# Kernel optimization log

Hardware: AMD Instinct MI355X
Metric: run time of the kernel (lower is better)

Reference implementation:

```python
import jax, jax.numpy as jnp
import numpy as np

H = 14
N = H * H
DIM = 768
INT = 5
LAM = 3.5


def fft_conv_grouped(x, w):
    # x: (B, g*in_c, N) real; w: (g, int_c, in_c, H, H//2+1) complex
    g, int_c, in_c = w.shape[:3]
    B = x.shape[0]
    xf = jnp.fft.rfftn(x.reshape(B, g, in_c, H, H), axes=(-2, -1), norm='ortho')
    yf = jnp.einsum('bgchf,gichf->bgihf', xf, w)
    y = jnp.fft.irfftn(yf, s=(H, H), axes=(-2, -1), norm='ortho')
    return y.reshape(B, g * int_c, N)


def soft(x, t):
    # sign(x) * relu(|x| - t)
    return jnp.sign(x) * jnp.maximum(jnp.abs(x) - t, 0.0)


def batch_norm(x, gamma, beta, eps=1e-5):
    # training-mode BatchNorm1d applied per channel over (B, N); x: (B, N, C)
    m = x.mean(axis=(0, 1))
    v = x.var(axis=(0, 1))
    return (x - m) * jax.lax.rsqrt(v + eps) * gamma + beta


def setup_inputs() -> dict:
    key = jax.random.key(0)
    ks = jax.random.split(key, 8)
    B = 32
    Hf = H // 2 + 1
    # kernel: init randn*0.06, then normalize_parameters()
    kr = jax.random.normal(ks[0], (DIM, INT, 1, H, Hf, 2), dtype=jnp.float32) * 0.06
    kc = kr[..., 0] + 1j * kr[..., 1]
    nrm = jnp.sqrt((jnp.abs(kc) ** 2).sum(axis=(2, 3, 4), keepdims=True) * 2.0 / H ** 2)
    kc = kc / nrm
    kernel = jnp.stack([jnp.real(kc), jnp.imag(kc)], axis=-1)
    # L buffer: update_L(lam=1) -> per-group max singular value of Gram kk
    kk = jnp.einsum('gichf,gjchf->gijhf', kc, jnp.conj(kc))
    sv = np.linalg.svd(np.asarray(jnp.transpose(kk, (0, 3, 4, 1, 2))), compute_uv=False)
    L = jnp.asarray(sv.reshape(DIM, -1).max(axis=-1), dtype=jnp.float32)
    hid = 4 * DIM
    return {
        'x': jax.random.normal(ks[1], (B, N, DIM), dtype=jnp.float32),
        'v_w': jax.random.normal(ks[2], (DIM, DIM), dtype=jnp.float32) * 0.02,
        'proj_w': jax.random.normal(ks[3], (DIM, DIM), dtype=jnp.float32) * 0.02,
        'proj_b': jnp.zeros((DIM,), dtype=jnp.float32),
        'kernel': kernel,
        'kernel2': jax.random.normal(ks[4], (DIM, 1, 1, H, Hf, 2), dtype=jnp.float32) * 0.02,
        'n1_g': jnp.ones((DIM,), dtype=jnp.float32),
        'n1_b': jnp.zeros((DIM,), dtype=jnp.float32),
        'n2_g': jnp.ones((DIM,), dtype=jnp.float32),
        'n2_b': jnp.zeros((DIM,), dtype=jnp.float32),
        'fc1_w': jax.random.normal(ks[5], (hid, DIM), dtype=jnp.float32) * 0.02,
        'fc1_b': jnp.zeros((hid,), dtype=jnp.float32),
        'fc2_w': jax.random.normal(ks[6], (DIM, hid), dtype=jnp.float32) * 0.02,
        'fc2_b': jnp.zeros((DIM,), dtype=jnp.float32),
        'L': L,
    }


def reference(x, v_w, proj_w, proj_b, kernel, kernel2, n1_g, n1_b, n2_g, n2_b, fc1_w, fc1_b, fc2_w, fc2_b, L):
    k = kernel[..., 0] + 1j * kernel[..., 1]                 # (g, int, 1, H, Hf)
    kk = jnp.einsum('gichf,gjchf->gijhf', k, jnp.conj(k))     # (g, int, int, H, Hf)
    vx = x @ v_w.T                                            # v Linear, no bias
    xc = jnp.swapaxes(vx, -2, -1)                             # (B, C, N)
    u = fft_conv_grouped(xc, k)                               # (B, g*int, N)
    Lv = jnp.repeat(L, INT)[None, :, None]                    # (1, g*int, 1)
    # ISTA: init soft-threshold then 3 gradient + shrink steps
    s = soft(u, LAM)
    for _ in range(3):
        s = s - (fft_conv_grouped(s, kk) - u) / Lv
        s = soft(s, LAM / Lv)
    # reconstruct with conjugate-transposed kernel, then mix with kernel2
    new = fft_conv_grouped(s, jnp.swapaxes(jnp.conj(k), 1, 2))  # (B, g, N)
    k2 = kernel2[..., 0] + 1j * kernel2[..., 1]
    new = fft_conv_grouped(new, k2)
    new = jnp.swapaxes(new, -2, -1)                           # (B, N, C)
    new = x + (batch_norm(new, n1_g, n1_b) @ proj_w.T + proj_b)
    h = jax.nn.gelu(batch_norm(new, n2_g, n2_b) @ fc1_w.T + fc1_b, approximate=False)
    return new + (h @ fc2_w.T + fc2_b)
```

## Files before the change

### kernel.cpp

```cpp
#include <hip/hip_runtime.h>
#include <cmath>

typedef unsigned short u16;
typedef __bf16 bf16x8 __attribute__((ext_vector_type(8)));
typedef float f32x4 __attribute__((ext_vector_type(4)));
typedef float float4v __attribute__((ext_vector_type(4)));
typedef u16 ushort4v __attribute__((ext_vector_type(4)));
typedef u16 ushort8v __attribute__((ext_vector_type(8)));

#define DIMC 768
#define NP 196
#define MTOT 6272
#define HIDC 3072
#define LAMC 3.5f

__device__ const float C14d[14] = {
  1.0f, 0.9009688679024191f, 0.6234898018587336f, 0.22252093395631445f,
  -0.22252093395631445f, -0.6234898018587336f, -0.9009688679024191f, -1.0f,
  -0.9009688679024191f, -0.6234898018587336f, -0.22252093395631445f,
  0.22252093395631445f, 0.6234898018587336f, 0.9009688679024191f
};
__device__ const float S14d[14] = {
  0.0f, 0.43388373911755823f, 0.7818314824680298f, 0.9749279121818236f,
  0.9749279121818236f, 0.7818314824680298f, 0.43388373911755823f, 0.0f,
  -0.43388373911755823f, -0.7818314824680298f, -0.9749279121818236f,
  -0.9749279121818236f, -0.7818314824680298f, -0.43388373911755823f
};

__device__ __forceinline__ u16 f2bf(float f) {
  unsigned u = __builtin_bit_cast(unsigned, f);
  unsigned r = u + 0x7FFFu + ((u >> 16) & 1u);
  return (u16)(r >> 16);
}

__device__ __forceinline__ size_t fidx(int m, int k, int K) {
  return ((size_t)(m >> 4) * (K >> 5) + (k >> 5)) * 512 +
         (size_t)((((k >> 3) & 3) * 16 + (m & 15)) * 8 + (k & 7));
}

__global__ __launch_bounds__(256) void prep_k(
    const float* __restrict__ v_w, const float* __restrict__ fc2w,
    const float* __restrict__ x,
    u16* __restrict__ vwf, u16* __restrict__ fc2f, u16* __restrict__ xf,
    u16* __restrict__ Ff, u16* __restrict__ Gf) {
  const int bid = blockIdx.x, t = threadIdx.x;
  if (bid < 378) {
    int idx = bid * 256 + t;
    if (idx < 50176) {
      int j = idx & 7, lane = (idx >> 3) & 63;
      int mk = idx >> 9, k0 = mk % 7, m0 = mk / 7;
      int s = m0 * 16 + (lane & 15);
      int q = k0 * 32 + (lane >> 4) * 8 + j;
      float v = 0.f;
      if (q < 196) {
        int kr = s >> 4, f = (s >> 1) & 7, r = q / 14, c = q % 14;
        int th = (kr * r + f * c) % 14;
        v = (s & 1) ? -S14d[th] : C14d[th];
      }
      Ff[idx] = f2bf(v);
    } else {
      int t2 = idx - 50176;
      int j = t2 & 7, lane = (t2 >> 3) & 63;
      int pk = t2 >> 9, k0 = pk % 7, p0 = pk / 7;
      int p = p0 * 16 + (lane & 15);
      int s = k0 * 32 + (lane >> 4) * 8 + j;
      float v = 0.f;
      if (p < 196) {
        int kr = s >> 4, f = (s >> 1) & 7, r = p / 14, c = p % 14;
        int th = (kr * r + f * c) % 14;
        float w = (f == 0 || f == 7) ? 1.f : 2.f;
        v = (w * (1.f / 196.f)) * ((s & 1) ? -S14d[th] : C14d[th]);
      }
      Gf[t2] = f2bf(v);
    }
    return;
  }
  const float* src; u16* dst; int idx, K;
  if (bid < 666)        { src = v_w;  dst = vwf;  idx = (bid - 378) * 256 + t;  K = DIMC; }
  else if (bid < 1818)  { src = fc2w; dst = fc2f; idx = (bid - 666) * 256 + t;  K = HIDC; }
  else                  { src = x;    dst = xf;   idx = (bid - 1818) * 256 + t; K = DIMC; }
  const int KC = K >> 5;
  int chunk = idx >> 6, l = idx & 63;
  int row = (chunk / KC) * 16 + (l & 15);
  int k0 = (chunk % KC) * 32 + (l >> 4) * 8;
  const float* sp = src + (size_t)row * K + k0;
  float4v f0 = *(const float4v*)sp;
  float4v f1 = *(const float4v*)(sp + 4);
  ushort8v o;
#pragma unroll
  for (int j = 0; j < 4; ++j) { o[j] = f2bf(f0[j]); o[j + 4] = f2bf(f1[j]); }
  *(ushort8v*)(dst + (size_t)idx * 8) = o;
}

template<int EPI>
__global__ __launch_bounds__(256, 3) void gemmw_k(
    const u16* __restrict__ Af, const u16* __restrict__ Bf,
    const float* __restrict__ bias, const float* __restrict__ res,
    void* __restrict__ Cp, int Nr, int Kr, int NB) {
  const int t = threadIdx.x, w = t >> 6, lane = t & 63;
  const int bid = blockIdx.x;
  const int xcd = bid & 7, j = bid >> 3;
  const int mt = xcd + 8 * (j / NB);
  if (mt >= 98) return;
  const int m0 = mt * 64;
  const int n0 = ((j % NB) * 4 + w) * 64;
  const int KC = Kr >> 5;
  const int l15 = lane & 15, l4 = lane >> 4;

  const u16* Ab = Af + ((size_t)(m0 >> 4) * KC) * 512 + lane * 8;
  const u16* Bb = Bf + ((size_t)(n0 >> 4) * KC) * 512 + lane * 8;

  f32x4 acc[4][4];
#pragma unroll
  for (int a = 0; a < 4; ++a)
#pragma unroll
    for (int b2 = 0; b2 < 4; ++b2) acc[a][b2] = (f32x4){0.f, 0.f, 0.f, 0.f};

  bf16x8 a0[4], b0[4], a1[4], b1[4];
#pragma unroll
  for (int mb = 0; mb < 4; ++mb) a0[mb] = *(const bf16x8*)(Ab + ((size_t)mb * KC) * 512);
#pragma unroll
  for (int nb = 0; nb < 4; ++nb) b0[nb] = *(const bf16x8*)(Bb + ((size_t)nb * KC) * 512);

  for (int kc = 0; kc < KC; kc += 2) {
#pragma unroll
    for (int mb = 0; mb < 4; ++mb)
      a1[mb] = *(const bf16x8*)(Ab + ((size_t)mb * KC + kc + 1) * 512);
#pragma unroll
    for (int nb = 0; nb < 4; ++nb)
      b1[nb] = *(const bf16x8*)(Bb + ((size_t)nb * KC + kc + 1) * 512);
    __builtin_amdgcn_s_setprio(1);
#pragma unroll
    for (int mb = 0; mb < 4; ++mb)
#pragma unroll
      for (int nb = 0; nb < 4; ++nb)
        acc[mb][nb] = __builtin_amdgcn_mfma_f32_16x16x32_bf16(a0[mb], b0[nb], acc[mb][nb], 0, 0, 0);
    __builtin_amdgcn_s_setprio(0);
    if (kc + 2 < KC) {
#pragma unroll
      for (int mb = 0; mb < 4; ++mb)
        a0[mb] = *(const bf16x8*)(Ab + ((size_t)mb * KC + kc + 2) * 512);
#pragma unroll
      for (int nb = 0; nb < 4; ++nb)
        b0[nb] = *(const bf16x8*)(Bb + ((size_t)nb * KC + kc + 2) * 512);
    }
    __builtin_amdgcn_s_setprio(1);
#pragma unroll
    for (int mb = 0; mb < 4; ++mb)
#pragma unroll
      for (int nb = 0; nb < 4; ++nb)
        acc[mb][nb] = __builtin_amdgcn_mfma_f32_16x16x32_bf16(a1[mb], b1[nb], acc[mb][nb], 0, 0, 0);
    __builtin_amdgcn_s_setprio(0);
  }

#pragma unroll
  for (int mb = 0; mb < 4; ++mb) {
#pragma unroll
    for (int nb = 0; nb < 4; ++nb) {
      int n = n0 + nb * 16 + l15;
      if (EPI == 0) {
        int m0r = m0 + mb * 16 + l4 * 4;
        int bb = m0r / 196, np0 = m0r - bb * 196;
        *(float4v*)&((float*)Cp)[((size_t)bb * DIMC + n) * 196 + np0] =
            (float4v){acc[mb][nb][0], acc[mb][nb][1], acc[mb][nb][2], acc[mb][nb][3]};
      } else {
#pragma unroll
        for (int r = 0; r < 4; ++r) {
          int m = m0 + mb * 16 + l4 * 4 + r;
          float v = acc[mb][nb][r];
          if (EPI == 1) {
            ((float*)Cp)[(size_t)m * Nr + n] = v + bias[n] + res[(size_t)m * Nr + n];
          } else {
            float vb = v + bias[n];
            float ge = 0.5f * vb * (1.f + erff(vb * 0.70710678118654752f));
            ((u16*)Cp)[fidx(m, n, Nr)] = f2bf(ge);
          }
        }
      }
    }
  }
}

__global__ __launch_bounds__(64) void checkmfma_k(
    const float* __restrict__ vxt, const float* __restrict__ kern,
    const u16* __restrict__ Ff, const u16* __restrict__ Gf,
    int* __restrict__ cnt, int* __restrict__ wl) {
  __shared__ float xf[16 * 228];
  const int lane = threadIdx.x;
  const int wgb = blockIdx.x;
  const int g = wgb >> 2, bhalf = (wgb >> 1) & 1, ihalf = wgb & 1;
  const int i0 = ihalf ? 3 : 0, ni = ihalf ? 2 : 3;
  const int tl = lane & 15, h = lane >> 4;
  const float* xbase = vxt + ((size_t)(bhalf * 16 + tl) * DIMC + g) * 196;

  bf16x8 Bx[7];
#pragma unroll
  for (int k0 = 0; k0 < 7; ++k0) {
    int q0 = k0 * 32 + h * 8;
    ushort8v tv;
    if (k0 < 6) {
      float4v f0 = *(const float4v*)(xbase + q0);
      float4v f1 = *(const float4v*)(xbase + q0 + 4);
#pragma unroll
      for (int j = 0; j < 4; ++j) { tv[j] = f2bf(f0[j]); tv[j + 4] = f2bf(f1[j]); }
    } else {
#pragma unroll
      for (int j = 0; j < 8; ++j) {
        int q = q0 + j;
        tv[j] = (q < 196) ? f2bf(xbase[q]) : (u16)0;
      }
    }
    Bx[k0] = __builtin_bit_cast(bf16x8, tv);
  }

  for (int m0 = 0; m0 < 14; ++m0) {
    f32x4 acc = (f32x4){0.f, 0.f, 0.f, 0.f};
#pragma unroll
    for (int k0 = 0; k0 < 7; ++k0) {
      bf16x8 Af = __builtin_bit_cast(bf16x8,
          *(const ushort8v*)(Ff + ((size_t)(m0 * 7 + k0) * 64 + lane) * 8));
      acc = __builtin_amdgcn_mfma_f32_16x16x32_bf16(Af, Bx[k0], acc, 0, 0, 0);
    }
    *(f32x4*)&xf[tl * 228 + m0 * 16 + h * 4] = acc;
  }

  bf16x8 By[3][7];
#pragma unroll
  for (int ii = 0; ii < 3; ++ii) {
    if (ii < ni) {
      const float* kb = kern + ((size_t)g * 5 + i0 + ii) * 224;
#pragma unroll
      for (int k0 = 0; k0 < 7; ++k0) {
        f32x4 x0 = *(const f32x4*)&xf[tl * 228 + k0 * 32 + h * 8];
        f32x4 x1 = *(const f32x4*)&xf[tl * 228 + k0 * 32 + h * 8 + 4];
        int mb = k0 * 16 + h * 4;
        float2 ka = *(const float2*)(kb + (mb + 0) * 2);
        float2 kc = *(const float2*)(kb + (mb + 1) * 2);
        float2 ke = *(const float2*)(kb + (mb + 2) * 2);
        float2 kg = *(const float2*)(kb + (mb + 3) * 2);
        ushort8v tv;
        tv[0] = f2bf(ka.x * x0[0] - ka.y * x0[1]);
        tv[1] = f2bf(ka.x * x0[1] + ka.y * x0[0]);
        tv[2] = f2bf(kc.x * x0[2] - kc.y * x0[3]);
        tv[3] = f2bf(kc.x * x0[3] + kc.y * x0[2]);
        tv[4] = f2bf(ke.x * x1[0] - ke.y * x1[1]);
        tv[5] = f2bf(ke.x * x1[1] + ke.y * x1[0]);
        tv[6] = f2bf(kg.x * x1[2] - kg.y * x1[3]);
        tv[7] = f2bf(kg.x * x1[3] + kg.y * x1[2]);
        By[ii][k0] = __builtin_bit_cast(bf16x8, tv);
      }
    }
  }

  float vmax = 0.f;
  for (int p0 = 0; p0 < 13; ++p0) {
    f32x4 a0 = (f32x4){0.f, 0.f, 0.f, 0.f};
    f32x4 a1 = a0, a2 = a0;
#pragma unroll
    for (int k0 = 0; k0 < 7; ++k0) {
      bf16x8 Ag = __builtin_bit_cast(bf16x8,
          *(const ushort8v*)(Gf + ((size_t)(p0 * 7 + k0) * 64 + lane) * 8));
      a0 = __builtin_amdgcn_mfma_f32_16x16x32_bf16(Ag, By[0][k0], a0, 0, 0, 0);
      a1 = __builtin_amdgcn_mfma_f32_16x16x32_bf16(Ag, By[1][k0], a1, 0, 0, 0);
      if (ni == 3)
        a2 = __builtin_amdgcn_mfma_f32_16x16x32_bf16(Ag, By[2][k0], a2, 0, 0, 0);
    }
#pragma unroll
    for (int r = 0; r < 4; ++r) {
      vmax = fmaxf(vmax, fabsf(a0[r]));
      vmax = fmaxf(vmax, fabsf(a1[r]));
      if (ni == 3) vmax = fmaxf(vmax, fabsf(a2[r]));
    }
  }
  vmax = fmaxf(vmax, __shfl_xor(vmax, 16));
  vmax = fmaxf(vmax, __shfl_xor(vmax, 32));
  if (lane < 16 && vmax > (LAMC - 0.1f)) {
    int idx = atomicAdd(cnt, 1);
    wl[idx] = g * 32 + bhalf * 16 + lane;
  }
}

__global__ __launch_bounds__(64) void slow_k(
    const float* __restrict__ vxt, const float* __restrict__ kern,
    const float* __restrict__ kern2, const float* __restrict__ Lbuf,
    const int* __restrict__ cnt, const int* __restrict__ wl,
    float* __restrict__ outp,
    float* __restrict__ tsum, float* __restrict__ tsq,
    unsigned* __restrict__ maskg, unsigned* __restrict__ bmask) {
  const int ntile = *cnt;
  if ((int)blockIdx.x >= ntile) return;
  const int t = threadIdx.x;
  __shared__ float TC[196], TSn[196];
  __shared__ float xs[196];
  __shared__ float t1R[112], t1I[112];
  __shared__ float t2R[112], t2I[112];
  __shared__ float zr[112], zi[112];
  __shared__ float kR[5][112], kI[5][112];
  __shared__ float uu[5][196];
  __shared__ float ss[5][196];
  __shared__ float k2R[112], k2I[112];

  for (int i = t; i < 196; i += 64) {
    int a = i / 14, c = i - (i / 14) * 14;
    int m = (a * c) % 14;
    TC[i] = C14d[m]; TSn[i] = S14d[m];
  }

  auto rowsFwd = [&](const float* xsrc) {
    for (int i = t; i < 112; i += 64) {
      int r = i >> 3, f = i & 7;
      const float* xp = xsrc + r * 14;
      const float* tc = &TC[f * 14]; const float* tsn = &TSn[f * 14];
      float ar = 0.f, ai = 0.f;
#pragma unroll
      for (int c = 0; c < 14; ++c) { float xv = xp[c]; ar += xv * tc[c]; ai -= xv * tsn[c]; }
      t1R[i] = ar; t1I[i] = ai;
    }
    __syncthreads();
  };
  auto colsFwd = [&](float* oR, float* oI) {
    for (int i = t; i < 112; i += 64) {
      int kr = i >> 3, f = i & 7;
      const float* tc = &TC[kr * 14]; const float* tsn = &TSn[kr * 14];
      float br = 0.f, bi = 0.f;
#pragma unroll
      for (int r = 0; r < 14; ++r) {
        float xr = t1R[r * 8 + f], xi = t1I[r * 8 + f];
        br += tc[r] * xr + tsn[r] * xi;
        bi += tc[r] * xi - tsn[r] * xr;
      }
      oR[i] = br; oI[i] = bi;
    }
    __syncthreads();
  };
  auto colsInv = [&]() {
    for (int i = t; i < 112; i += 64) {
      int r = i >> 3, f = i & 7;
      const float* tc = &TC[r * 14]; const float* tsn = &TSn[r * 14];
      float br = 0.f, bi = 0.f;
#pragma unroll
      for (int kr = 0; kr < 14; ++kr) {
        float xr = t1R[kr * 8 + f], xi = t1I[kr * 8 + f];
        br += tc[kr] * xr - tsn[kr] * xi;
        bi += tc[kr] * xi + tsn[kr] * xr;
      }
      t2R[i] = br; t2I[i] = bi;
    }
    __syncthreads();
  };
  auto rowVal = [&](int r, int c) -> float {
    const float* pR = &t2R[r * 8]; const float* pI = &t2I[r * 8];
    float v = pR[0] + ((c & 1) ? -pR[7] : pR[7]);
    float s2 = 0.f;
#pragma unroll
    for (int f = 1; f < 7; ++f) s2 += pR[f] * TC[f * 14 + c] - pI[f] * TSn[f * 14 + c];
    return (v + 2.f * s2) * (1.0f / 196.0f);
  };

  for (int widx = blockIdx.x; widx < ntile; widx += gridDim.x) {
    const int tile = wl[widx];
    const int g = tile >> 5, b = tile & 31;
    __syncthreads();
    for (int i = t; i < 560; i += 64) {
      int ii = i / 112, p = i - ii * 112;
      const float* kp = kern + ((size_t)g * 5 + ii) * 224 + p * 2;
      kR[ii][p] = kp[0]; kI[ii][p] = kp[1];
    }
    for (int i = t; i < 196; i += 64) xs[i] = vxt[((size_t)b * DIMC + g) * 196 + i];
    for (int i = t; i < 112; i += 64) {
      k2R[i] = kern2[(size_t)g * 224 + i * 2];
      k2I[i] = kern2[(size_t)g * 224 + i * 2 + 1];
    }
    __syncthreads();

    rowsFwd(xs);
    colsFwd(zr, zi);
    for (int ii = 0; ii < 5; ++ii) {
      for (int i = t; i < 112; i += 64) {
        float a = kR[ii][i], b2 = kI[ii][i];
        t1R[i] = a * zr[i] - b2 * zi[i];
        t1I[i] = a * zi[i] + b2 * zr[i];
      }
      __syncthreads();
      colsInv();
      for (int i = t; i < 196; i += 64) uu[ii][i] = rowVal(i / 14, i - (i / 14) * 14);
      __syncthreads();
    }

    const float invL = 1.0f / Lbuf[g];
    const float thr = LAMC * invL;
    {
      float* up = &uu[0][0];
      float* sp = &ss[0][0];
      for (int i = t; i < 980; i += 64) {
        float v = up[i];
        float a = fabsf(v) - LAMC;
        sp[i] = a > 0.f ? copysignf(a, v) : 0.f;
      }
    }
    __syncthreads();

    for (int iter = 0; iter < 4; ++iter) {
      for (int i = t; i < 112; i += 64) { zr[i] = 0.f; zi[i] = 0.f; }
      __syncthreads();
      for (int ii = 0; ii < 5; ++ii) {
        rowsFwd(&ss[ii][0]);
        colsFwd(t2R, t2I);
        for (int i = t; i < 112; i += 64) {
          float a = kR[ii][i], b2 = kI[ii][i];
          zr[i] += a * t2R[i] + b2 * t2I[i];
          zi[i] += a * t2I[i] - b2 * t2R[i];
        }
        __syncthreads();
      }
      if (iter == 3) break;
      for (int ii = 0; ii < 5; ++ii) {
        for (int i = t; i < 112; i += 64) {
          float a = kR[ii][i], b2 = kI[ii][i];
          t1R[i] = a * zr[i] - b2 * zi[i];
          t1I[i] = a * zi[i] + b2 * zr[i];
        }
        __syncthreads();
        colsInv();
        for (int i = t; i < 196; i += 64) {
          float v = rowVal(i / 14, i - (i / 14) * 14);
          float sv = ss[ii][i] - (v - uu[ii][i]) * invL;
          float aa = fabsf(sv) - thr;
          ss[ii][i] = aa > 0.f ? copysignf(aa, sv) : 0.f;
        }
        __syncthreads();
      }
    }

    if (t < 28) {
      int kr = t >> 1, f = (t & 1) * 7;
      int d = kr * 8 + f;
      int srci = ((14 - kr) % 14) * 8 + f;
      float pr = 0.5f * (zr[d] + zr[srci]);
      float pi = 0.5f * (zi[d] - zi[srci]);
      zr[d] = pr; zi[d] = pi;
    }
    __syncthreads();
    for (int i = t; i < 112; i += 64) {
      float a = k2R[i], b2 = k2I[i];
      t1R[i] = a * zr[i] - b2 * zi[i];
      t1I[i] = a * zi[i] + b2 * zr[i];
    }
    __syncthreads();
    colsInv();
    float sacc = 0.f, qacc = 0.f;
    for (int i = t; i < 196; i += 64) {
      float v = rowVal(i / 14, i - (i / 14) * 14);
      outp[((size_t)(b * 196 + i)) * DIMC + g] = v;
      sacc += v; qacc += v * v;
    }
#pragma unroll
    for (int off = 32; off; off >>= 1) {
      sacc += __shfl_xor(sacc, off);
      qacc += __shfl_xor(qacc, off);
    }
    if (t == 0) {
      tsum[tile] = sacc; tsq[tile] = qacc;
      atomicOr(&maskg[g], 1u << b);
      atomicOr(bmask, 1u << b);
    }
  }
}

__global__ __launch_bounds__(256) void stats1c0_k(
    const float* __restrict__ tsum, const float* __restrict__ tsq,
    const unsigned* __restrict__ maskg,
    const float* __restrict__ gam, const float* __restrict__ bet,
    const float* __restrict__ projw, const float* __restrict__ pb,
    float* __restrict__ sc1, float* __restrict__ c0) {
  __shared__ float sh1s[768];
  const int t = threadIdx.x;
  for (int c = t; c < DIMC; c += 256) {
    unsigned mask = maskg[c];
    float S = 0.f, Q = 0.f;
    if (mask) {
      for (int b = 0; b < 32; ++b)
        if ((mask >> b) & 1) { S += tsum[c * 32 + b]; Q += tsq[c * 32 + b]; }
    }
    float m = S * (1.0f / 6272.0f);
    float v = fmaxf(Q * (1.0f / 6272.0f) - m * m, 0.f);
    float rs = rsqrtf(v + 1e-5f);
    float sc = gam[c] * rs;
    sh1s[c] = bet[c] - m * sc;
    if (blockIdx.x == 0) sc1[c] = sc;
  }
  __syncthreads();
  int n = blockIdx.x * 256 + t;
  const float* row = projw + (size_t)n * DIMC;
  float s = 0.f;
  for (int g = 0; g < DIMC; g += 4) {
    float4v r = *(const float4v*)(row + g);
    s += r[0] * sh1s[g] + r[1] * sh1s[g + 1] + r[2] * sh1s[g + 2] + r[3] * sh1s[g + 3];
  }
  c0[n] = s + pb[n];
}

__global__ __launch_bounds__(256) void bnb_k(
    const float* __restrict__ x, const float* __restrict__ c0,
    const float* __restrict__ sc1, const unsigned* __restrict__ maskg,
    const unsigned* __restrict__ bmask, const float* __restrict__ newm,
    const float* __restrict__ projw,
    float* __restrict__ new2, u16* __restrict__ n2f,
    float* __restrict__ part) {
  const int jb = blockIdx.x, b = blockIdx.y, t = threadIdx.x;
  __shared__ unsigned gm[24];
  __shared__ float c0s[768];
  const bool hasb = ((*bmask >> b) & 1u) != 0u;
  if (t < 24) {
    unsigned w = 0;
    if (hasb)
      for (int j2 = 0; j2 < 32; ++j2) w |= ((maskg[t * 32 + j2] >> b) & 1u) << j2;
    gm[t] = w;
  }
  for (int c = t; c < 768; c += 256) c0s[c] = c0[c];
  __syncthreads();

  float S0 = 0, S1 = 0, S2 = 0, Q0 = 0, Q1 = 0, Q2 = 0;
  for (int mr = 0; mr < 7; ++mr) {
    int m = b * 196 + jb * 7 + mr;
    size_t row = (size_t)m * DIMC;
#pragma unroll
    for (int j2 = 0; j2 < 3; ++j2) {
      int n = t + j2 * 256;
      float v = x[row + n] + c0s[n];
      if (hasb) {
        for (int w = 0; w < 24; ++w) {
          unsigned bits = gm[w];
          while (bits) {
            int g = w * 32 + __builtin_ctz(bits);
            bits &= bits - 1;
            v += sc1[g] * newm[row + g] * projw[(size_t)n * DIMC + g];
          }
        }
      }
      new2[row + n] = v;
      n2f[fidx(m, n, DIMC)] = f2bf(v);
      if (j2 == 0) { S0 += v; Q0 += v * v; }
      else if (j2 == 1) { S1 += v; Q1 += v * v; }
      else { S2 += v; Q2 += v * v; }
    }
  }
  float* p = part + (size_t)(b * 28 + jb) * 1536;
  p[t] = S0; p[t + 256] = S1; p[t + 512] = S2;
  p[768 + t] = Q0; p[768 + 256 + t] = Q1; p[768 + 512 + t] = Q2;
}

__global__ __launch_bounds__(256) void red2_k(const float* __restrict__ part,
                                              float* __restrict__ part2) {
  int slot = blockIdx.x * 256 + threadIdx.x;
  int b = blockIdx.y;
  float s = 0.f;
  const float* p = part + (size_t)(b * 28) * 1536 + slot;
  for (int jb = 0; jb < 28; ++jb) s += p[(size_t)jb * 1536];
  part2[(size_t)b * 1536 + slot] = s;
}

__global__ __launch_bounds__(256) void stats2fin_k(const float* __restrict__ part2,
    const float* __restrict__ gam, const float* __restrict__ bet,
    float* __restrict__ scale, float* __restrict__ shift) {
  int c = blockIdx.x * 256 + threadIdx.x;
  float S = 0.f, Q = 0.f;
  for (int b = 0; b < 32; ++b) {
    S += part2[(size_t)b * 1536 + c];
    Q += part2[(size_t)b * 1536 + 768 + c];
  }
  float m = S * (1.0f / 6272.0f);
  float v = fmaxf(Q * (1.0f / 6272.0f) - m * m, 0.f);
  float rs = rsqrtf(v + 1e-5f);
  float sc = gam[c] * rs;
  scale[c] = sc;
  shift[c] = bet[c] - m * sc;
}

__global__ __launch_bounds__(256) void foldfc1_k(const float* __restrict__ fc1w,
    const float* __restrict__ fc1b, const float* __restrict__ sc2,
    const float* __restrict__ sh2, u16* __restrict__ fc1s,
    float* __restrict__ d0) {
  const int bid = blockIdx.x, t = threadIdx.x;
  if (bid < 12) {
    int n = bid * 256 + t;
    const float* row = fc1w + (size_t)n * DIMC;
    float s = 0.f;
    for (int k = 0; k < DIMC; k += 4) {
      float4v r = *(const float4v*)(row + k);
      float4v h = *(const float4v*)(sh2 + k);
      s += r[0] * h[0] + r[1] * h[1] + r[2] * h[2] + r[3] * h[3];
    }
    d0[n] = s + fc1b[n];
  } else {
    int idx = (bid - 12) * 256 + t;
    int chunk = idx >> 6, l = idx & 63;
    int n = (chunk / 24) * 16 + (l & 15);
    int k0 = (chunk % 24) * 32 + (l >> 4) * 8;
    const float* sp = fc1w + (size_t)n * DIMC + k0;
    float4v f0 = *(const float4v*)sp;
    float4v f1 = *(const float4v*)(sp + 4);
    float4v s0 = *(const float4v*)(sc2 + k0);
    float4v s1 = *(const float4v*)(sc2 + k0 + 4);
    f0 = f0 * s0; f1 = f1 * s1;
    ushort8v o;
#pragma unroll
    for (int j = 0; j < 4; ++j) { o[j] = f2bf(f0[j]); o[j + 4] = f2bf(f1[j]); }
    *(ushort8v*)(fc1s + (size_t)idx * 8) = o;
  }
}

extern "C" void kernel_launch(void* const* d_in, const int* in_sizes, int n_in,
                              void* d_out, int out_size, void* d_ws, size_t ws_size,
                              hipStream_t stream) {
  (void)in_sizes; (void)n_in; (void)out_size;
  const float* x      = (const float*)d_in[0];
  const float* v_w    = (const float*)d_in[1];
  const float* proj_w = (const float*)d_in[2];
  const float* proj_b = (const float*)d_in[3];
  const float* kern   = (const float*)d_in[4];
  const float* kern2  = (const float*)d_in[5];
  const float* n1g    = (const float*)d_in[6];
  const float* n1b    = (const float*)d_in[7];
  const float* n2g    = (const float*)d_in[8];
  const float* n2b    = (const float*)d_in[9];
  const float* fc1w   = (const float*)d_in[10];
  const float* fc1b   = (const float*)d_in[11];
  const float* fc2w   = (const float*)d_in[12];
  const float* fc2b   = (const float*)d_in[13];
  const float* Lb     = (const float*)d_in[14];
  float* out = (float*)d_out;

  char* ws = (char*)d_ws;
  size_t o = 0;
  auto alloc = [&](size_t bytes) { size_t r = o; o += (bytes + 255) & ~(size_t)255; return r; };
  u16*   vwf    = (u16*)(ws + alloc(589824 * 2));
  u16*   fc2f   = (u16*)(ws + alloc(2359296 * 2));
  u16*   fc1s   = (u16*)(ws + alloc(2359296 * 2));
  u16*   Ffb    = (u16*)(ws + alloc(50176 * 2));
  u16*   Gfb    = (u16*)(ws + alloc(46592 * 2));
  float* sc1    = (float*)(ws + alloc(768 * 4));
  float* sc2    = (float*)(ws + alloc(768 * 4));
  float* sh2    = (float*)(ws + alloc(768 * 4));
  float* c0     = (float*)(ws + alloc(768 * 4));
  float* d0     = (float*)(ws + alloc(3072 * 4));
  float* part   = (float*)(ws + alloc((size_t)896 * 1536 * 4));
  float* part2  = (float*)(ws + alloc((size_t)32 * 1536 * 4));
  char*  zblk   = (char*)(ws + alloc(4096));
  int*      cnt   = (int*)zblk;
  unsigned* bmask = (unsigned*)(zblk + 4);
  unsigned* maskg = (unsigned*)(zblk + 8);
  int*   wl     = (int*)(ws + alloc(49152 * 4));
  float* tsum   = (float*)(ws + alloc(24576 * 4));
  float* tsq    = (float*)(ws + alloc(24576 * 4));
  u16*   xf     = (u16*)(ws + alloc((size_t)MTOT * DIMC * 2));
  u16*   n2f    = (u16*)(ws + alloc((size_t)MTOT * DIMC * 2));
  float* vxt    = (float*)(ws + alloc((size_t)MTOT * DIMC * 4));
  float* newm   = (float*)(ws + alloc((size_t)MTOT * DIMC * 4));
  float* new2   = (float*)(ws + alloc((size_t)MTOT * DIMC * 4));
  u16*   hbf    = (u16*)vxt;
  if (ws_size < o) return;

  hipMemsetAsync(zblk, 0, 4096, stream);

  prep_k<<<4170, 256, 0, stream>>>(v_w, fc2w, x, vwf, fc2f, xf, Ffb, Gfb);
  gemmw_k<0><<<312, 256, 0, stream>>>(xf, vwf, nullptr, nullptr, vxt, DIMC, DIMC, 3);
  checkmfma_k<<<3072, 64, 0, stream>>>(vxt, kern, Ffb, Gfb, cnt, wl);
  slow_k<<<1024, 64, 0, stream>>>(vxt, kern, kern2, Lb, cnt, wl, newm,
                                  tsum, tsq, maskg, bmask);
  stats1c0_k<<<3, 256, 0, stream>>>(tsum, tsq, maskg, n1g, n1b, proj_w, proj_b, sc1, c0);
  bnb_k<<<dim3(28, 32), 256, 0, stream>>>(x, c0, sc1, maskg, bmask, newm, proj_w,
                                          new2, n2f, part);
  red2_k<<<dim3(6, 32), 256, 0, stream>>>(part, part2);
  stats2fin_k<<<3, 256, 0, stream>>>(part2, n2g, n2b, sc2, sh2);
  foldfc1_k<<<1164, 256, 0, stream>>>(fc1w, fc1b, sc2, sh2, fc1s, d0);
  gemmw_k<2><<<1248, 256, 0, stream>>>(n2f, fc1s, d0, nullptr, hbf, HIDC, DIMC, 12);
  gemmw_k<1><<<312, 256, 0, stream>>>(hbf, fc2f, fc2b, new2, out, DIMC, HIDC, 3);
}
```

Measured before the change: 294.4 us.

## Split screening kernel into shared forward-DFT pass and per-channel screen pass

The fused screening kernel is split in two. xf_k computes the forward DFT of each (group, batch-half) tile once and writes it to a global buffer. screen_k then runs one small block per output channel, building its kernel-multiplied operand and doing the inverse DFT with paired MFMA accumulators. This removes the duplicated forward transform that each channel-half block used to compute, lowers register pressure, and spreads the work over more blocks. In exchange it adds a global write and repeated reads of the frequency-domain tile. The worklist may also collect more duplicate entries, since up to five blocks can now flag the same row.

```diff
diff --git a/kernel.cpp b/kernel.cpp
--- a/kernel.cpp
+++ b/kernel.cpp
@@ -181,15 +181,12 @@
   }
 }
 
-__global__ __launch_bounds__(64) void checkmfma_k(
-    const float* __restrict__ vxt, const float* __restrict__ kern,
-    const u16* __restrict__ Ff, const u16* __restrict__ Gf,
-    int* __restrict__ cnt, int* __restrict__ wl) {
-  __shared__ float xf[16 * 228];
+__global__ __launch_bounds__(64) void xf_k(
+    const float* __restrict__ vxt, const u16* __restrict__ Ff,
+    float* __restrict__ xfg) {
   const int lane = threadIdx.x;
   const int wgb = blockIdx.x;
-  const int g = wgb >> 2, bhalf = (wgb >> 1) & 1, ihalf = wgb & 1;
-  const int i0 = ihalf ? 3 : 0, ni = ihalf ? 2 : 3;
+  const int g = wgb >> 1, bhalf = wgb & 1;
   const int tl = lane & 15, h = lane >> 4;
   const float* xbase = vxt + ((size_t)(bhalf * 16 + tl) * DIMC + g) * 196;
 
@@ -213,6 +210,7 @@
     Bx[k0] = __builtin_bit_cast(bf16x8, tv);
   }
 
+  float* xo = xfg + (size_t)wgb * (16 * 224);
   for (int m0 = 0; m0 < 14; ++m0) {
     f32x4 acc = (f32x4){0.f, 0.f, 0.f, 0.f};
 #pragma unroll
@@ -221,57 +219,75 @@
           *(const ushort8v*)(Ff + ((size_t)(m0 * 7 + k0) * 64 + lane) * 8));
       acc = __builtin_amdgcn_mfma_f32_16x16x32_bf16(Af, Bx[k0], acc, 0, 0, 0);
     }
-    *(f32x4*)&xf[tl * 228 + m0 * 16 + h * 4] = acc;
-  }
-
-  bf16x8 By[3][7];
-#pragma unroll
-  for (int ii = 0; ii < 3; ++ii) {
-    if (ii < ni) {
-      const float* kb = kern + ((size_t)g * 5 + i0 + ii) * 224;
-#pragma unroll
-      for (int k0 = 0; k0 < 7; ++k0) {
-        f32x4 x0 = *(const f32x4*)&xf[tl * 228 + k0 * 32 + h * 8];
-        f32x4 x1 = *(const f32x4*)&xf[tl * 228 + k0 * 32 + h * 8 + 4];
-        int mb = k0 * 16 + h * 4;
-        float2 ka = *(const float2*)(kb + (mb + 0) * 2);
-        float2 kc = *(const float2*)(kb + (mb + 1) * 2);
-        float2 ke = *(const float2*)(kb + (mb + 2) * 2);
-        float2 kg = *(const float2*)(kb + (mb + 3) * 2);
-        ushort8v tv;
-        tv[0] = f2bf(ka.x * x0[0] - ka.y * x0[1]);
-        tv[1] = f2bf(ka.x * x0[1] + ka.y * x0[0]);
-        tv[2] = f2bf(kc.x * x0[2] - kc.y * x0[3]);
-        tv[3] = f2bf(kc.x * x0[3] + kc.y * x0[2]);
-        tv[4] = f2bf(ke.x * x1[0] - ke.y * x1[1]);
-        tv[5] = f2bf(ke.x * x1[1] + ke.y * x1[0]);
-        tv[6] = f2bf(kg.x * x1[2] - kg.y * x1[3]);
-        tv[7] = f2bf(kg.x * x1[3] + kg.y * x1[2]);
-        By[ii][k0] = __builtin_bit_cast(bf16x8, tv);
-      }
-    }
+    *(f32x4*)&xo[tl * 224 + m0 * 16 + h * 4] = acc;
+  }
+}
+
+__global__ __launch_bounds__(64) void screen_k(
+    const float* __restrict__ xfg, const float* __restrict__ kern,
+    const u16* __restrict__ Gf, int* __restrict__ cnt, int* __restrict__ wl) {
+  const int lane = threadIdx.x;
+  const int bid = blockIdx.x;
+  const int gb = bid / 5, i = bid - gb * 5;
+  const int g = gb >> 1, bhalf = gb & 1;
+  const int tl = lane & 15, h = lane >> 4;
+  const float* xo = xfg + (size_t)gb * (16 * 224);
+  const float* kb = kern + ((size_t)g * 5 + i) * 224;
+
+  bf16x8 By[7];
+#pragma unroll
+  for (int k0 = 0; k0 < 7; ++k0) {
+    f32x4 x0 = *(const f32x4*)&xo[tl * 224 + k0 * 32 + h * 8];
+    f32x4 x1 = *(const f32x4*)&xo[tl * 224 + k0 * 32 + h * 8 + 4];
+    int mb = k0 * 16 + h * 4;
+    float2 ka = *(const float2*)(kb + (mb + 0) * 2);
+    float2 kc = *(const float2*)(kb + (mb + 1) * 2);
+    float2 ke = *(const float2*)(kb + (mb + 2) * 2);
+    float2 kg = *(const float2*)(kb + (mb + 3) * 2);
+    ushort8v tv;
+    tv[0] = f2bf(ka.x * x0[0] - ka.y * x0[1]);
+    tv[1] = f2bf(ka.x * x0[1] + ka.y * x0[0]);
+    tv[2] = f2bf(kc.x * x0[2] - kc.y * x0[3]);
+    tv[3] = f2bf(kc.x * x0[3] + kc.y * x0[2]);
+    tv[4] = f2bf(ke.x * x1[0] - ke.y * x1[1]);
+    tv[5] = f2bf(ke.x * x1[1] + ke.y * x1[0]);
+    tv[6] = f2bf(kg.x * x1[2] - kg.y * x1[3]);
+    tv[7] = f2bf(kg.x * x1[3] + kg.y * x1[2]);
+    By[k0] = __builtin_bit_cast(bf16x8, tv);
   }
 
   float vmax = 0.f;
-  for (int p0 = 0; p0 < 13; ++p0) {
+  for (int pp = 0; pp < 6; ++pp) {
+    int p0 = pp * 2;
     f32x4 a0 = (f32x4){0.f, 0.f, 0.f, 0.f};
-    f32x4 a1 = a0, a2 = a0;
+    f32x4 a1 = a0;
 #pragma unroll
     for (int k0 = 0; k0 < 7; ++k0) {
-      bf16x8 Ag = __builtin_bit_cast(bf16x8,
+      bf16x8 Ag0 = __builtin_bit_cast(bf16x8,
           *(const ushort8v*)(Gf + ((size_t)(p0 * 7 + k0) * 64 + lane) * 8));
-      a0 = __builtin_amdgcn_mfma_f32_16x16x32_bf16(Ag, By[0][k0], a0, 0, 0, 0);
-      a1 = __builtin_amdgcn_mfma_f32_16x16x32_bf16(Ag, By[1][k0], a1, 0, 0, 0);
-      if (ni == 3)
-        a2 = __builtin_amdgcn_mfma_f32_16x16x32_bf16(Ag, By[2][k0], a2, 0, 0, 0);
+      bf16x8 Ag1 = __builtin_bit_cast(bf16x8,
+          *(const ushort8v*)(Gf + ((size_t)((p0 + 1) * 7 + k0) * 64 + lane) * 8));
+      a0 = __builtin_amdgcn_mfma_f32_16x16x32_bf16(Ag0, By[k0], a0, 0, 0, 0);
+      a1 = __builtin_amdgcn_mfma_f32_16x16x32_bf16(Ag1, By[k0], a1, 0, 0, 0);
     }
 #pragma unroll
     for (int r = 0; r < 4; ++r) {
       vmax = fmaxf(vmax, fabsf(a0[r]));
       vmax = fmaxf(vmax, fabsf(a1[r]));
-      if (ni == 3) vmax = fmaxf(vmax, fabsf(a2[r]));
-    }
-  }
+    }
+  }
+  {
+    f32x4 a0 = (f32x4){0.f, 0.f, 0.f, 0.f};
+#pragma unroll
+    for (int k0 = 0; k0 < 7; ++k0) {
+      bf16x8 Ag = __builtin_bit_cast(bf16x8,
+          *(const ushort8v*)(Gf + ((size_t)(12 * 7 + k0) * 64 + lane) * 8));
+      a0 = __builtin_amdgcn_mfma_f32_16x16x32_bf16(Ag, By[k0], a0, 0, 0, 0);
+    }
+#pragma unroll
+    for (int r = 0; r < 4; ++r) vmax = fmaxf(vmax, fabsf(a0[r]));
+  }
+
   vmax = fmaxf(vmax, __shfl_xor(vmax, 16));
   vmax = fmaxf(vmax, __shfl_xor(vmax, 32));
   if (lane < 16 && vmax > (LAMC - 0.1f)) {
@@ -650,9 +666,10 @@
   int*      cnt   = (int*)zblk;
   unsigned* bmask = (unsigned*)(zblk + 4);
   unsigned* maskg = (unsigned*)(zblk + 8);
-  int*   wl     = (int*)(ws + alloc(49152 * 4));
+  int*   wl     = (int*)(ws + alloc(131072 * 4));
   float* tsum   = (float*)(ws + alloc(24576 * 4));
   float* tsq    = (float*)(ws + alloc(24576 * 4));
+  float* xfg    = (float*)(ws + alloc((size_t)1536 * 16 * 224 * 4));
   u16*   xf     = (u16*)(ws + alloc((size_t)MTOT * DIMC * 2));
   u16*   n2f    = (u16*)(ws + alloc((size_t)MTOT * DIMC * 2));
   float* vxt    = (float*)(ws + alloc((size_t)MTOT * DIMC * 4));
@@ -665,7 +682,8 @@
 
   prep_k<<<4170, 256, 0, stream>>>(v_w, fc2w, x, vwf, fc2f, xf, Ffb, Gfb);
   gemmw_k<0><<<312, 256, 0, stream>>>(xf, vwf, nullptr, nullptr, vxt, DIMC, DIMC, 3);
-  checkmfma_k<<<3072, 64, 0, stream>>>(vxt, kern, Ffb, Gfb, cnt, wl);
+  xf_k<<<1536, 64, 0, stream>>>(vxt, Ffb, xfg);
+  screen_k<<<7680, 64, 0, stream>>>(xfg, kern, Gfb, cnt, wl);
   slow_k<<<1024, 64, 0, stream>>>(vxt, kern, kern2, Lb, cnt, wl, newm,
                                   tsum, tsq, maskg, bmask);
   stats1c0_k<<<3, 256, 0, stream>>>(tsum, tsq, maskg, n1g, n1b, proj_w, proj_b, sc1, c0);
```

Result: faster. 284.3 us (-3.4%).
